# Performance work log

Hardware: AMD Instinct MI355X
Metric: run time of the kernel (lower is better)

The kernel has to match this reference:

```python
import jax, jax.numpy as jnp
import numpy as np


def setup_inputs() -> dict:
    key = jax.random.key(0)
    ks = jax.random.split(key, 5)
    B, T, S, D = 4, 32, 320, 768
    return {
        "x": jax.random.normal(ks[0], (B, T, S, D), dtype=jnp.float32),
        "qkv_w": jax.random.normal(ks[1], (D, 3 * D), dtype=jnp.float32) * 0.02,
        "qkv_b": jax.random.normal(ks[2], (3 * D,), dtype=jnp.float32) * 0.02,
        "out_w": jax.random.normal(ks[3], (D, D), dtype=jnp.float32) * 0.02,
        "out_b": jax.random.normal(ks[4], (D,), dtype=jnp.float32) * 0.02,
        "n_latents": 64,
        "n_heads": 12,
    }


def reference(x, qkv_w, qkv_b, out_w, out_b, n_latents, n_heads):
    B, T, S, D = x.shape
    H = n_heads
    hd = D // H
    scale = 1.0 / jnp.sqrt(jnp.asarray(hd, dtype=x.dtype))

    # qkv projection: [B,T,S,3D]
    qkv = jnp.einsum('btsd,de->btse', x, qkv_w) + qkv_b
    q, k, v = jnp.split(qkv, 3, axis=-1)
    # [B,T,S,H,hd]
    q = q.reshape(B, T, S, H, hd)
    k = k.reshape(B, T, S, H, hd)
    v = v.reshape(B, T, S, H, hd)

    # block-sparse mask: latent queries (rows < n_latents) cannot attend to
    # patch keys (cols >= n_latents); everything else allowed
    rows = jnp.arange(S) < n_latents          # latent query rows
    cols = jnp.arange(S) >= n_latents         # patch key cols
    allow = ~(rows[:, None] & cols[None, :])  # [S,S] bool

    # attention scores [B,T,H,Sq,Sk]
    scores = jnp.einsum('btqhd,btkhd->bthqk', q, k) * scale
    scores = jnp.where(allow, scores, -jnp.inf)
    attn = jax.nn.softmax(scores, axis=-1)

    y = jnp.einsum('bthqk,btkhd->btqhd', attn, v).reshape(B, T, S, D)
    return jnp.einsum('btsd,de->btse', y, out_w) + out_b
```

## Files before the change

kernel.cpp:

```cpp
#include <hip/hip_runtime.h>

typedef __attribute__((ext_vector_type(8))) short bf16x8;
typedef __attribute__((ext_vector_type(4))) float f32x4;
typedef __attribute__((ext_vector_type(16))) float f32x16;
typedef __attribute__((address_space(1))) void gvoid_t;
typedef __attribute__((address_space(3))) void lvoid_t;

#define DEVI __device__ __forceinline__

DEVI unsigned short f2bf(float f) {
    unsigned int u = __builtin_bit_cast(unsigned int, f);
    u += 0x7fffu + ((u >> 16) & 1u);
    return (unsigned short)(u >> 16);
}

DEVI unsigned cvt_pk_bf16(float a, float b) {
    unsigned r;
    asm("v_cvt_pk_bf16_f32 %0, %1, %2" : "=v"(r) : "v"(a), "v"(b));
    return r;
}

DEVI f32x4 mfma16(bf16x8 a, bf16x8 b, f32x4 c) {
    return __builtin_amdgcn_mfma_f32_16x16x32_bf16(a, b, c, 0, 0, 0);
}

__global__ void k_convert(const float* __restrict__ in, unsigned short* __restrict__ out, int n8) {
    int i = blockIdx.x * 256 + threadIdx.x;
    if (i >= n8) return;
    const float4* p = (const float4*)in + (size_t)i * 2;
    float4 a = p[0], b = p[1];
    uint4 o;
    o.x = f2bf(a.x) | ((unsigned)f2bf(a.y) << 16);
    o.y = f2bf(a.z) | ((unsigned)f2bf(a.w) << 16);
    o.z = f2bf(b.x) | ((unsigned)f2bf(b.y) << 16);
    o.w = f2bf(b.z) | ((unsigned)f2bf(b.w) << 16);
    *((uint4*)out + i) = o;
}

__global__ void k_transpose(const float* __restrict__ w, unsigned short* __restrict__ wt, int K, int N) {
    __shared__ float tile[32][33];
    int n0 = blockIdx.x * 32, k0 = blockIdx.y * 32;
    int tx = threadIdx.x, ty = threadIdx.y;
#pragma unroll
    for (int r = 0; r < 32; r += 8)
        tile[ty + r][tx] = w[(size_t)(k0 + ty + r) * N + n0 + tx];
    __syncthreads();
#pragma unroll
    for (int r = 0; r < 32; r += 8)
        wt[(size_t)(n0 + ty + r) * K + k0 + tx] = f2bf(tile[tx][ty + r]);
}

template <bool OUT_BF16>
__global__ __launch_bounds__(512, 2) void k_gemm256(const unsigned short* __restrict__ A,
                                                    const unsigned short* __restrict__ Bt,
                                                    const float* __restrict__ bias,
                                                    void* __restrict__ out,
                                                    int M, int N, int K) {
    __shared__ unsigned short smem[65536];

    const int tid = threadIdx.x;
    const int nwg = gridDim.x, bid = blockIdx.x;
    const int q8 = nwg >> 3, r8 = nwg & 7;
    const int xcd = bid & 7, lid = bid >> 3;
    const int swz = ((xcd < r8) ? xcd * (q8 + 1) : r8 * (q8 + 1) + (xcd - r8) * q8) + lid;
    const int ntn = N >> 8;
    const int bm = swz / ntn, bn = swz % ntn;

    const int lane = tid & 63, wid = tid >> 6;
    const int wr = wid >> 2, wc = wid & 3;
    const int lr = lane & 15, lg = lane >> 4;
    const int cswz = (lr & 7) << 3;
    const int col0 = (lg * 8) ^ cswz;

    const int NT = K >> 6;

    const int srowl = tid >> 3;
    const int scole = ((tid & 7) ^ (srowl & 7)) << 3;
    const unsigned short* aSrc = A  + (size_t)(bm * 256 + srowl) * K + scole;
    const unsigned short* bSrc = Bt + (size_t)(bn * 256 + srowl) * K + scole;

#define STG(matOff, srcBase, qq, koff, bufw)                                              \
    __builtin_amdgcn_global_load_lds((gvoid_t*)((srcBase) + (size_t)(qq) * 64 * K + (koff)), \
        (lvoid_t*)(smem + (matOff) + (bufw) * 16384 + (qq) * 4096 + tid * 8), 16, 0, 0)

    f32x4 acc[8][4];
#pragma unroll
    for (int i = 0; i < 8; ++i)
#pragma unroll
        for (int j = 0; j < 4; ++j) acc[i][j] = (f32x4){0.f, 0.f, 0.f, 0.f};

    {
        const int k1 = (NT > 1) ? 64 : 0;
        STG(0, aSrc, 0, 0, 0); STG(0, aSrc, 1, 0, 0); STG(0, aSrc, 2, 0, 0); STG(0, aSrc, 3, 0, 0);
        STG(32768, bSrc, 0, 0, 0); STG(32768, bSrc, 1, 0, 0); STG(32768, bSrc, 2, 0, 0); STG(32768, bSrc, 3, 0, 0);
        STG(0, aSrc, 0, k1, 1); STG(0, aSrc, 2, k1, 1);
        asm volatile("s_waitcnt vmcnt(2)" ::: "memory");
        __builtin_amdgcn_s_barrier();
    }

#pragma unroll 1
    for (int t = 0; t < NT; ++t) {
        const int bufR = t & 1, bufW = bufR ^ 1;
        const int ko1 = (t + 1 < NT) ? (t + 1) * 64 : 0;
        const int ko2 = (t + 2 < NT) ? (t + 2) * 64 : 0;
        const unsigned short* abuf = smem + bufR * 16384;
        const unsigned short* bbuf = smem + 32768 + bufR * 16384;
        bf16x8 af[4][2], b01[2][2], b23[2][2];

#pragma unroll
        for (int mf = 0; mf < 4; ++mf)
#pragma unroll
            for (int kk = 0; kk < 2; ++kk)
                af[mf][kk] = *(const bf16x8*)(abuf + (wr * 128 + mf * 16 + lr) * 64 + (col0 ^ (kk * 32)));
#pragma unroll
        for (int j = 0; j < 2; ++j)
#pragma unroll
            for (int kk = 0; kk < 2; ++kk)
                b01[j][kk] = *(const bf16x8*)(bbuf + (wc * 64 + j * 16 + lr) * 64 + (col0 ^ (kk * 32)));
        STG(32768, bSrc, 0, ko1, bufW); STG(32768, bSrc, 1, ko1, bufW);
        __builtin_amdgcn_s_barrier();
        asm volatile("s_waitcnt lgkmcnt(0)" ::: "memory");
        __builtin_amdgcn_sched_barrier(0);
        __builtin_amdgcn_s_setprio(1);
#pragma unroll
        for (int mf = 0; mf < 4; ++mf)
#pragma unroll
            for (int j = 0; j < 2; ++j)
#pragma unroll
                for (int kk = 0; kk < 2; ++kk)
                    acc[mf][j] = mfma16(af[mf][kk], b01[j][kk], acc[mf][j]);
        __builtin_amdgcn_s_setprio(0);
        __builtin_amdgcn_s_barrier();

#pragma unroll
        for (int j = 0; j < 2; ++j)
#pragma unroll
            for (int kk = 0; kk < 2; ++kk)
                b23[j][kk] = *(const bf16x8*)(bbuf + (wc * 64 + (2 + j) * 16 + lr) * 64 + (col0 ^ (kk * 32)));
        STG(32768, bSrc, 2, ko1, bufW); STG(32768, bSrc, 3, ko1, bufW);
        __builtin_amdgcn_s_barrier();
        asm volatile("s_waitcnt lgkmcnt(0)" ::: "memory");
        __builtin_amdgcn_sched_barrier(0);
        __builtin_amdgcn_s_setprio(1);
#pragma unroll
        for (int mf = 0; mf < 4; ++mf)
#pragma unroll
            for (int j = 0; j < 2; ++j)
#pragma unroll
                for (int kk = 0; kk < 2; ++kk)
                    acc[mf][2 + j] = mfma16(af[mf][kk], b23[j][kk], acc[mf][2 + j]);
        __builtin_amdgcn_s_setprio(0);
        __builtin_amdgcn_s_barrier();

#pragma unroll
        for (int mf = 0; mf < 4; ++mf)
#pragma unroll
            for (int kk = 0; kk < 2; ++kk)
                af[mf][kk] = *(const bf16x8*)(abuf + (wr * 128 + 64 + mf * 16 + lr) * 64 + (col0 ^ (kk * 32)));
        STG(0, aSrc, 1, ko1, bufW); STG(0, aSrc, 3, ko1, bufW);
        __builtin_amdgcn_s_barrier();
        asm volatile("s_waitcnt lgkmcnt(0)" ::: "memory");
        __builtin_amdgcn_sched_barrier(0);
        __builtin_amdgcn_s_setprio(1);
#pragma unroll
        for (int mf = 0; mf < 4; ++mf)
#pragma unroll
            for (int j = 0; j < 2; ++j)
#pragma unroll
                for (int kk = 0; kk < 2; ++kk)
                    acc[4 + mf][2 + j] = mfma16(af[mf][kk], b23[j][kk], acc[4 + mf][2 + j]);
        __builtin_amdgcn_s_setprio(0);
        __builtin_amdgcn_s_barrier();

        STG(0, aSrc, 0, ko2, bufR); STG(0, aSrc, 2, ko2, bufR);
        __builtin_amdgcn_s_setprio(1);
#pragma unroll
        for (int mf = 0; mf < 4; ++mf)
#pragma unroll
            for (int j = 0; j < 2; ++j)
#pragma unroll
                for (int kk = 0; kk < 2; ++kk)
                    acc[4 + mf][j] = mfma16(af[mf][kk], b01[j][kk], acc[4 + mf][j]);
        __builtin_amdgcn_s_setprio(0);
        asm volatile("s_waitcnt vmcnt(2)" ::: "memory");
        __builtin_amdgcn_s_barrier();
    }
#undef STG

    asm volatile("s_waitcnt vmcnt(0)" ::: "memory");
    float bv[4];
#pragma unroll
    for (int nf = 0; nf < 4; ++nf)
        bv[nf] = bias[bn * 256 + wc * 64 + nf * 16 + lr];

    if (OUT_BF16) {
        unsigned short* ebuf = smem + wid * 8192;
#pragma unroll
        for (int h = 0; h < 2; ++h) {
#pragma unroll
            for (int mf4 = 0; mf4 < 4; ++mf4) {
                int mf = h * 4 + mf4;
#pragma unroll
                for (int nf = 0; nf < 4; ++nf)
#pragma unroll
                    for (int i = 0; i < 4; ++i)
                        ebuf[(mf4 * 16 + lg * 4 + i) * 72 + nf * 16 + lr] = f2bf(acc[mf][nf][i] + bv[nf]);
            }
            asm volatile("s_waitcnt lgkmcnt(0)" ::: "memory");
            __builtin_amdgcn_sched_barrier(0);
#pragma unroll
            for (int ps = 0; ps < 8; ++ps) {
                int rl = ps * 8 + (lane >> 3), ck = lane & 7;
                uint4 vv = *(const uint4*)&ebuf[rl * 72 + ck * 8];
                int grow = bm * 256 + wr * 128 + h * 64 + rl;
                int gcol = bn * 256 + wc * 64 + ck * 8;
                *(uint4*)&((unsigned short*)out)[(size_t)grow * N + gcol] = vv;
            }
            asm volatile("s_waitcnt lgkmcnt(0)" ::: "memory");
            __builtin_amdgcn_sched_barrier(0);
        }
    } else {
        float* ebuf = (float*)smem + wid * 4096;
#pragma unroll
        for (int qq = 0; qq < 4; ++qq) {
#pragma unroll
            for (int m2 = 0; m2 < 2; ++m2) {
                int mf = qq * 2 + m2;
#pragma unroll
                for (int nf = 0; nf < 4; ++nf)
#pragma unroll
                    for (int i = 0; i < 4; ++i)
                        ebuf[(m2 * 16 + lg * 4 + i) * 68 + nf * 16 + lr] = acc[mf][nf][i] + bv[nf];
            }
            asm volatile("s_waitcnt lgkmcnt(0)" ::: "memory");
            __builtin_amdgcn_sched_barrier(0);
#pragma unroll
            for (int ps = 0; ps < 8; ++ps) {
                int rl = ps * 4 + (lane >> 4), ck = lane & 15;
                uint4 vv = *(const uint4*)&ebuf[rl * 68 + ck * 4];
                int grow = bm * 256 + wr * 128 + qq * 32 + rl;
                int gcol = bn * 256 + wc * 64 + ck * 4;
                *(uint4*)&((float*)out)[(size_t)grow * N + gcol] = vv;
            }
            asm volatile("s_waitcnt lgkmcnt(0)" ::: "memory");
            __builtin_amdgcn_sched_barrier(0);
        }
    }
}

__global__ __launch_bounds__(640) void k_attn4(const unsigned short* __restrict__ qkv,
                                               unsigned short* __restrict__ y) {
    int bt = blockIdx.x / 12, h = blockIdx.x % 12;
    const unsigned short* Qg = qkv + (size_t)bt * 320 * 2304 + h * 64;
    const unsigned short* Kg = Qg + 768;
    const unsigned short* Vg = Qg + 1536;

    __shared__ unsigned short Vt[10 * 64 * 40];

    int tid = threadIdx.x, w = tid >> 6, l = tid & 63;
    int q = l & 31, hh = l >> 5;
    int q0 = w * 32;
    int ntile = (w < 2) ? 2 : 10;

    {
        int k = tid >> 1;
        int tt = k >> 5, sk = k & 31;
        int d0 = (tid & 1) * 32;
        const unsigned short* src = Vg + (size_t)k * 2304 + d0;
#pragma unroll
        for (int c = 0; c < 4; ++c) {
            union { uint4 u; unsigned short s[8]; } vv;
            vv.u = *(const uint4*)(src + c * 8);
#pragma unroll
            for (int j = 0; j < 8; ++j) {
                int d = d0 + c * 8 + j;
                Vt[(tt * 64 + d) * 40 + (sk ^ (((d >> 3) & 3) << 3))] = vv.s[j];
            }
        }
    }

    bf16x8 qf[4];
#pragma unroll
    for (int c = 0; c < 4; ++c)
        qf[c] = *(const bf16x8*)(Qg + (size_t)(q0 + q) * 2304 + c * 16 + hh * 8);

    f32x16 o0 = (f32x16)0.f, o1 = (f32x16)0.f;
    float m = -3e38f, lsum = 0.f;
    const float SC = 0.125f * 1.44269504089f;

    bf16x8 kfA[4], kfB[4];
    auto loadK = [&](bf16x8 (&kf)[4], int tt) {
#pragma unroll
        for (int c = 0; c < 4; ++c)
            kf[c] = *(const bf16x8*)(Kg + (size_t)(tt * 32 + q) * 2304 + c * 16 + hh * 8);
    };
    loadK(kfA, 0);

    __syncthreads();

    auto process = [&](int t, bf16x8 (&kf)[4]) {
        f32x16 sacc = (f32x16)0.f;
#pragma unroll
        for (int c = 0; c < 4; ++c)
            sacc = __builtin_amdgcn_mfma_f32_32x32x16_bf16(kf[c], qf[c], sacc, 0, 0, 0);

        float p[16];
#pragma unroll
        for (int r = 0; r < 16; ++r) p[r] = sacc[r] * SC;
        float tm = fmaxf(
            fmaxf(fmaxf(fmaxf(p[0], p[1]), fmaxf(p[2], p[3])),
                  fmaxf(fmaxf(p[4], p[5]), fmaxf(p[6], p[7]))),
            fmaxf(fmaxf(fmaxf(p[8], p[9]), fmaxf(p[10], p[11])),
                  fmaxf(fmaxf(p[12], p[13]), fmaxf(p[14], p[15]))));
        tm = fmaxf(tm, __shfl_xor(tm, 32));
        if (!__all(tm <= m + 8.f)) {
            float mn = fmaxf(m, tm);
            float al = __builtin_amdgcn_exp2f(m - mn);
            lsum *= al;
#pragma unroll
            for (int r = 0; r < 16; ++r) { o0[r] *= al; o1[r] *= al; }
            m = mn;
        }
#pragma unroll
        for (int r = 0; r < 16; ++r) p[r] = __builtin_amdgcn_exp2f(p[r] - m);
        float rs =
            ((p[0] + p[1]) + (p[2] + p[3])) + ((p[4] + p[5]) + (p[6] + p[7])) +
            (((p[8] + p[9]) + (p[10] + p[11])) + ((p[12] + p[13]) + (p[14] + p[15])));
        lsum += rs;

        unsigned a0 = cvt_pk_bf16(p[0], p[1]);
        unsigned a1 = cvt_pk_bf16(p[2], p[3]);
        unsigned b0 = cvt_pk_bf16(p[4], p[5]);
        unsigned b1 = cvt_pk_bf16(p[6], p[7]);
        asm("v_permlane32_swap_b32 %0, %1" : "+v"(a0), "+v"(b0));
        asm("v_permlane32_swap_b32 %0, %1" : "+v"(a1), "+v"(b1));
        unsigned c0 = cvt_pk_bf16(p[8], p[9]);
        unsigned c1 = cvt_pk_bf16(p[10], p[11]);
        unsigned d0 = cvt_pk_bf16(p[12], p[13]);
        unsigned d1 = cvt_pk_bf16(p[14], p[15]);
        asm("v_permlane32_swap_b32 %0, %1" : "+v"(c0), "+v"(d0));
        asm("v_permlane32_swap_b32 %0, %1" : "+v"(c1), "+v"(d1));
        union { unsigned u[4]; bf16x8 v; } pf0, pf1;
        pf0.u[0] = a0; pf0.u[1] = a1; pf0.u[2] = b0; pf0.u[3] = b1;
        pf1.u[0] = c0; pf1.u[1] = c1; pf1.u[2] = d0; pf1.u[3] = d1;

        const unsigned short* vt = Vt + t * 2560;
        {
            int d = q;
            int sw = (d >> 3) & 3;
            bf16x8 va0 = *(const bf16x8*)&vt[d * 40 + ((0 + hh) ^ sw) * 8];
            bf16x8 va1 = *(const bf16x8*)&vt[d * 40 + ((2 + hh) ^ sw) * 8];
            o0 = __builtin_amdgcn_mfma_f32_32x32x16_bf16(va0, pf0.v, o0, 0, 0, 0);
            o0 = __builtin_amdgcn_mfma_f32_32x32x16_bf16(va1, pf1.v, o0, 0, 0, 0);
        }
        {
            int d = 32 + q;
            int sw = (d >> 3) & 3;
            bf16x8 va0 = *(const bf16x8*)&vt[d * 40 + ((0 + hh) ^ sw) * 8];
            bf16x8 va1 = *(const bf16x8*)&vt[d * 40 + ((2 + hh) ^ sw) * 8];
            o1 = __builtin_amdgcn_mfma_f32_32x32x16_bf16(va0, pf0.v, o1, 0, 0, 0);
            o1 = __builtin_amdgcn_mfma_f32_32x32x16_bf16(va1, pf1.v, o1, 0, 0, 0);
        }
    };

    for (int t = 0; t < ntile; t += 2) {
        loadK(kfB, t + 1);
        process(t, kfA);
        loadK(kfA, (t + 2 < 10) ? (t + 2) : 8);
        process(t + 1, kfB);
    }

    lsum += __shfl_xor(lsum, 32);
    float inv = 1.f / lsum;
    unsigned short* yp = y + (size_t)(bt * 320 + q0 + q) * 768 + h * 64;
#pragma unroll
    for (int r = 0; r < 16; r += 2) {
        int dr = (r & 3) + 8 * (r >> 2) + 4 * hh;
        *(unsigned*)(yp + dr) =
            (unsigned)f2bf(o0[r] * inv) | ((unsigned)f2bf(o0[r + 1] * inv) << 16);
        *(unsigned*)(yp + 32 + dr) =
            (unsigned)f2bf(o1[r] * inv) | ((unsigned)f2bf(o1[r + 1] * inv) << 16);
    }
}

extern "C" void kernel_launch(void* const* d_in, const int* in_sizes, int n_in,
                              void* d_out, int out_size, void* d_ws, size_t ws_size,
                              hipStream_t stream) {
    const float* x     = (const float*)d_in[0];
    const float* qkv_w = (const float*)d_in[1];
    const float* qkv_b = (const float*)d_in[2];
    const float* out_w = (const float*)d_in[3];
    const float* out_b = (const float*)d_in[4];

    const int M = 40960;
    unsigned short* xb  = (unsigned short*)d_ws;
    unsigned short* w1t = xb + (size_t)M * 768;
    unsigned short* w2t = w1t + (size_t)2304 * 768;
    unsigned short* qkv = w2t + (size_t)768 * 768;
    unsigned short* yb  = qkv + (size_t)M * 2304;

    k_convert<<<(M * 768 / 8 + 255) / 256, 256, 0, stream>>>(x, xb, M * 768 / 8);
    k_transpose<<<dim3(2304 / 32, 768 / 32), dim3(32, 8), 0, stream>>>(qkv_w, w1t, 768, 2304);
    k_transpose<<<dim3(768 / 32, 768 / 32), dim3(32, 8), 0, stream>>>(out_w, w2t, 768, 768);

    k_gemm256<true><<<(M / 256) * (2304 / 256), 512, 0, stream>>>(xb, w1t, qkv_b, (void*)qkv, M, 2304, 768);
    k_attn4<<<128 * 12, 640, 0, stream>>>(qkv, yb);
    k_gemm256<false><<<(M / 256) * (768 / 256), 512, 0, stream>>>(yb, w2t, out_b, d_out, M, 768, 768);
}
```

Before: 378.6 us.

## Drop mid-loop barriers in GEMM and prepack K tiles for attention

The GEMM main loop no longer places a workgroup barrier between each MFMA quarter. It splits the LDS fragment loads into halves with partial lgkmcnt waits, so MFMAs can start while the remaining fragments arrive, and it keeps a single vmcnt(0) plus barrier at the end of each iteration. A new k_kpack kernel copies K into a per-(bt,head,tile) contiguous layout in the now-unused x buffer, so the attention kernel's K fragment loads become contiguous 16-byte loads instead of loads strided by 2304. This trades an extra launch and roughly 60MB of extra memory traffic for better-coalesced K reads and fewer GEMM synchronisations. The stricter vmcnt(0) wait also reduces prefetch overlap slightly.

```diff
diff --git a/kernel.cpp b/kernel.cpp
--- a/kernel.cpp
+++ b/kernel.cpp
@@ -7,6 +7,7 @@
 typedef __attribute__((address_space(3))) void lvoid_t;
 
 #define DEVI __device__ __forceinline__
+#define SB __builtin_amdgcn_sched_barrier(0)
 
 DEVI unsigned short f2bf(float f) {
     unsigned int u = __builtin_bit_cast(unsigned int, f);
@@ -50,6 +51,18 @@
         wt[(size_t)(n0 + ty + r) * K + k0 + tx] = f2bf(tile[tx][ty + r]);
 }
 
+__global__ __launch_bounds__(256) void k_kpack(const unsigned short* __restrict__ qkv,
+                                               unsigned short* __restrict__ kp) {
+    int bht = blockIdx.x;
+    int t = bht % 10, bh = bht / 10;
+    int h = bh % 12, bt = bh / 12;
+    int c = threadIdx.x >> 6, l = threadIdx.x & 63;
+    const unsigned short* src = qkv + (size_t)(bt * 320 + t * 32 + (l & 31)) * 2304
+                                + 768 + h * 64 + c * 16 + (l >> 5) * 8;
+    uint4 v = *(const uint4*)src;
+    *(uint4*)(kp + ((size_t)bht * 4 + c) * 512 + l * 8) = v;
+}
+
 template <bool OUT_BF16>
 __global__ __launch_bounds__(512, 2) void k_gemm256(const unsigned short* __restrict__ A,
                                                     const unsigned short* __restrict__ Bt,
@@ -82,6 +95,8 @@
 #define STG(matOff, srcBase, qq, koff, bufw)                                              \
     __builtin_amdgcn_global_load_lds((gvoid_t*)((srcBase) + (size_t)(qq) * 64 * K + (koff)), \
         (lvoid_t*)(smem + (matOff) + (bufw) * 16384 + (qq) * 4096 + tid * 8), 16, 0, 0)
+#define LDA(mf, base, rowoff, kk) \
+    *(const bf16x8*)((base) + ((rowoff) + (mf) * 16 + lr) * 64 + (col0 ^ ((kk) * 32)))
 
     f32x4 acc[8][4];
 #pragma unroll
@@ -105,89 +120,125 @@
         const int ko2 = (t + 2 < NT) ? (t + 2) * 64 : 0;
         const unsigned short* abuf = smem + bufR * 16384;
         const unsigned short* bbuf = smem + 32768 + bufR * 16384;
-        bf16x8 af[4][2], b01[2][2], b23[2][2];
-
+        bf16x8 afv[4][2], b01[2][2], b23[2][2];
+
+#pragma unroll
+        for (int j = 0; j < 2; ++j)
+#pragma unroll
+            for (int kk = 0; kk < 2; ++kk)
+                b01[j][kk] = LDA(j, bbuf, wc * 64, kk);
+#pragma unroll
+        for (int mf = 0; mf < 2; ++mf)
+#pragma unroll
+            for (int kk = 0; kk < 2; ++kk)
+                afv[mf][kk] = LDA(mf, abuf, wr * 128, kk);
+        SB;
+#pragma unroll
+        for (int mf = 2; mf < 4; ++mf)
+#pragma unroll
+            for (int kk = 0; kk < 2; ++kk)
+                afv[mf][kk] = LDA(mf, abuf, wr * 128, kk);
+        SB;
+        STG(32768, bSrc, 0, ko1, bufW); STG(32768, bSrc, 1, ko1, bufW);
+        asm volatile("s_waitcnt lgkmcnt(4)" ::: "memory"); SB;
+        __builtin_amdgcn_s_setprio(1);
+#pragma unroll
+        for (int mf = 0; mf < 2; ++mf)
+#pragma unroll
+            for (int j = 0; j < 2; ++j)
+#pragma unroll
+                for (int kk = 0; kk < 2; ++kk)
+                    acc[mf][j] = mfma16(afv[mf][kk], b01[j][kk], acc[mf][j]);
+        __builtin_amdgcn_s_setprio(0);
+        asm volatile("s_waitcnt lgkmcnt(0)" ::: "memory"); SB;
+        __builtin_amdgcn_s_setprio(1);
+#pragma unroll
+        for (int mf = 2; mf < 4; ++mf)
+#pragma unroll
+            for (int j = 0; j < 2; ++j)
+#pragma unroll
+                for (int kk = 0; kk < 2; ++kk)
+                    acc[mf][j] = mfma16(afv[mf][kk], b01[j][kk], acc[mf][j]);
+        __builtin_amdgcn_s_setprio(0);
+
+#pragma unroll
+        for (int kk = 0; kk < 2; ++kk)
+            b23[0][kk] = LDA(2, bbuf, wc * 64, kk);
+        SB;
+#pragma unroll
+        for (int kk = 0; kk < 2; ++kk)
+            b23[1][kk] = LDA(3, bbuf, wc * 64, kk);
+        SB;
+        STG(32768, bSrc, 2, ko1, bufW); STG(32768, bSrc, 3, ko1, bufW);
+        asm volatile("s_waitcnt lgkmcnt(2)" ::: "memory"); SB;
+        __builtin_amdgcn_s_setprio(1);
 #pragma unroll
         for (int mf = 0; mf < 4; ++mf)
 #pragma unroll
             for (int kk = 0; kk < 2; ++kk)
-                af[mf][kk] = *(const bf16x8*)(abuf + (wr * 128 + mf * 16 + lr) * 64 + (col0 ^ (kk * 32)));
-#pragma unroll
-        for (int j = 0; j < 2; ++j)
-#pragma unroll
-            for (int kk = 0; kk < 2; ++kk)
-                b01[j][kk] = *(const bf16x8*)(bbuf + (wc * 64 + j * 16 + lr) * 64 + (col0 ^ (kk * 32)));
-        STG(32768, bSrc, 0, ko1, bufW); STG(32768, bSrc, 1, ko1, bufW);
+                acc[mf][2] = mfma16(afv[mf][kk], b23[0][kk], acc[mf][2]);
+        __builtin_amdgcn_s_setprio(0);
+        asm volatile("s_waitcnt lgkmcnt(0)" ::: "memory"); SB;
+        __builtin_amdgcn_s_setprio(1);
+#pragma unroll
+        for (int mf = 0; mf < 4; ++mf)
+#pragma unroll
+            for (int kk = 0; kk < 2; ++kk)
+                acc[mf][3] = mfma16(afv[mf][kk], b23[1][kk], acc[mf][3]);
+        __builtin_amdgcn_s_setprio(0);
+
+#pragma unroll
+        for (int mf = 0; mf < 2; ++mf)
+#pragma unroll
+            for (int kk = 0; kk < 2; ++kk)
+                afv[mf][kk] = LDA(mf, abuf, wr * 128 + 64, kk);
+        SB;
+#pragma unroll
+        for (int mf = 2; mf < 4; ++mf)
+#pragma unroll
+            for (int kk = 0; kk < 2; ++kk)
+                afv[mf][kk] = LDA(mf, abuf, wr * 128 + 64, kk);
+        SB;
+        STG(0, aSrc, 1, ko1, bufW); STG(0, aSrc, 3, ko1, bufW);
+        asm volatile("s_waitcnt lgkmcnt(4)" ::: "memory"); SB;
+        __builtin_amdgcn_s_setprio(1);
+#pragma unroll
+        for (int mf = 0; mf < 2; ++mf)
+#pragma unroll
+            for (int j = 0; j < 2; ++j)
+#pragma unroll
+                for (int kk = 0; kk < 2; ++kk)
+                    acc[4 + mf][2 + j] = mfma16(afv[mf][kk], b23[j][kk], acc[4 + mf][2 + j]);
+        __builtin_amdgcn_s_setprio(0);
+        asm volatile("s_waitcnt lgkmcnt(0)" ::: "memory"); SB;
+        __builtin_amdgcn_s_setprio(1);
+#pragma unroll
+        for (int mf = 2; mf < 4; ++mf)
+#pragma unroll
+            for (int j = 0; j < 2; ++j)
+#pragma unroll
+                for (int kk = 0; kk < 2; ++kk)
+                    acc[4 + mf][2 + j] = mfma16(afv[mf][kk], b23[j][kk], acc[4 + mf][2 + j]);
+        __builtin_amdgcn_s_setprio(0);
+
+        __builtin_amdgcn_s_setprio(1);
+#pragma unroll
+        for (int mf = 0; mf < 4; ++mf)
+#pragma unroll
+            for (int j = 0; j < 2; ++j)
+#pragma unroll
+                for (int kk = 0; kk < 2; ++kk)
+                    acc[4 + mf][j] = mfma16(afv[mf][kk], b01[j][kk], acc[4 + mf][j]);
+        __builtin_amdgcn_s_setprio(0);
+        asm volatile("s_waitcnt vmcnt(0)" ::: "memory");
         __builtin_amdgcn_s_barrier();
-        asm volatile("s_waitcnt lgkmcnt(0)" ::: "memory");
-        __builtin_amdgcn_sched_barrier(0);
-        __builtin_amdgcn_s_setprio(1);
-#pragma unroll
-        for (int mf = 0; mf < 4; ++mf)
-#pragma unroll
-            for (int j = 0; j < 2; ++j)
-#pragma unroll
-                for (int kk = 0; kk < 2; ++kk)
-                    acc[mf][j] = mfma16(af[mf][kk], b01[j][kk], acc[mf][j]);
-        __builtin_amdgcn_s_setprio(0);
-        __builtin_amdgcn_s_barrier();
-
-#pragma unroll
-        for (int j = 0; j < 2; ++j)
-#pragma unroll
-            for (int kk = 0; kk < 2; ++kk)
-                b23[j][kk] = *(const bf16x8*)(bbuf + (wc * 64 + (2 + j) * 16 + lr) * 64 + (col0 ^ (kk * 32)));
-        STG(32768, bSrc, 2, ko1, bufW); STG(32768, bSrc, 3, ko1, bufW);
-        __builtin_amdgcn_s_barrier();
-        asm volatile("s_waitcnt lgkmcnt(0)" ::: "memory");
-        __builtin_amdgcn_sched_barrier(0);
-        __builtin_amdgcn_s_setprio(1);
-#pragma unroll
-        for (int mf = 0; mf < 4; ++mf)
-#pragma unroll
-            for (int j = 0; j < 2; ++j)
-#pragma unroll
-                for (int kk = 0; kk < 2; ++kk)
-                    acc[mf][2 + j] = mfma16(af[mf][kk], b23[j][kk], acc[mf][2 + j]);
-        __builtin_amdgcn_s_setprio(0);
-        __builtin_amdgcn_s_barrier();
-
-#pragma unroll
-        for (int mf = 0; mf < 4; ++mf)
-#pragma unroll
-            for (int kk = 0; kk < 2; ++kk)
-                af[mf][kk] = *(const bf16x8*)(abuf + (wr * 128 + 64 + mf * 16 + lr) * 64 + (col0 ^ (kk * 32)));
-        STG(0, aSrc, 1, ko1, bufW); STG(0, aSrc, 3, ko1, bufW);
-        __builtin_amdgcn_s_barrier();
-        asm volatile("s_waitcnt lgkmcnt(0)" ::: "memory");
-        __builtin_amdgcn_sched_barrier(0);
-        __builtin_amdgcn_s_setprio(1);
-#pragma unroll
-        for (int mf = 0; mf < 4; ++mf)
-#pragma unroll
-            for (int j = 0; j < 2; ++j)
-#pragma unroll
-                for (int kk = 0; kk < 2; ++kk)
-                    acc[4 + mf][2 + j] = mfma16(af[mf][kk], b23[j][kk], acc[4 + mf][2 + j]);
-        __builtin_amdgcn_s_setprio(0);
-        __builtin_amdgcn_s_barrier();
-
         STG(0, aSrc, 0, ko2, bufR); STG(0, aSrc, 2, ko2, bufR);
-        __builtin_amdgcn_s_setprio(1);
-#pragma unroll
-        for (int mf = 0; mf < 4; ++mf)
-#pragma unroll
-            for (int j = 0; j < 2; ++j)
-#pragma unroll
-                for (int kk = 0; kk < 2; ++kk)
-                    acc[4 + mf][j] = mfma16(af[mf][kk], b01[j][kk], acc[4 + mf][j]);
-        __builtin_amdgcn_s_setprio(0);
-        asm volatile("s_waitcnt vmcnt(2)" ::: "memory");
-        __builtin_amdgcn_s_barrier();
     }
 #undef STG
+#undef LDA
 
     asm volatile("s_waitcnt vmcnt(0)" ::: "memory");
+    __syncthreads();
     float bv[4];
 #pragma unroll
     for (int nf = 0; nf < 4; ++nf)
@@ -206,8 +257,7 @@
                     for (int i = 0; i < 4; ++i)
                         ebuf[(mf4 * 16 + lg * 4 + i) * 72 + nf * 16 + lr] = f2bf(acc[mf][nf][i] + bv[nf]);
             }
-            asm volatile("s_waitcnt lgkmcnt(0)" ::: "memory");
-            __builtin_amdgcn_sched_barrier(0);
+            asm volatile("s_waitcnt lgkmcnt(0)" ::: "memory"); SB;
 #pragma unroll
             for (int ps = 0; ps < 8; ++ps) {
                 int rl = ps * 8 + (lane >> 3), ck = lane & 7;
@@ -216,8 +266,7 @@
                 int gcol = bn * 256 + wc * 64 + ck * 8;
                 *(uint4*)&((unsigned short*)out)[(size_t)grow * N + gcol] = vv;
             }
-            asm volatile("s_waitcnt lgkmcnt(0)" ::: "memory");
-            __builtin_amdgcn_sched_barrier(0);
+            asm volatile("s_waitcnt lgkmcnt(0)" ::: "memory"); SB;
         }
     } else {
         float* ebuf = (float*)smem + wid * 4096;
@@ -232,8 +281,7 @@
                     for (int i = 0; i < 4; ++i)
                         ebuf[(m2 * 16 + lg * 4 + i) * 68 + nf * 16 + lr] = acc[mf][nf][i] + bv[nf];
             }
-            asm volatile("s_waitcnt lgkmcnt(0)" ::: "memory");
-            __builtin_amdgcn_sched_barrier(0);
+            asm volatile("s_waitcnt lgkmcnt(0)" ::: "memory"); SB;
 #pragma unroll
             for (int ps = 0; ps < 8; ++ps) {
                 int rl = ps * 4 + (lane >> 4), ck = lane & 15;
@@ -242,18 +290,18 @@
                 int gcol = bn * 256 + wc * 64 + ck * 4;
                 *(uint4*)&((float*)out)[(size_t)grow * N + gcol] = vv;
             }
-            asm volatile("s_waitcnt lgkmcnt(0)" ::: "memory");
-            __builtin_amdgcn_sched_barrier(0);
-        }
-    }
-}
-
-__global__ __launch_bounds__(640) void k_attn4(const unsigned short* __restrict__ qkv,
+            asm volatile("s_waitcnt lgkmcnt(0)" ::: "memory"); SB;
+        }
+    }
+}
+
+__global__ __launch_bounds__(640) void k_attn5(const unsigned short* __restrict__ qkv,
+                                               const unsigned short* __restrict__ kp,
                                                unsigned short* __restrict__ y) {
     int bt = blockIdx.x / 12, h = blockIdx.x % 12;
     const unsigned short* Qg = qkv + (size_t)bt * 320 * 2304 + h * 64;
-    const unsigned short* Kg = Qg + 768;
     const unsigned short* Vg = Qg + 1536;
+    const unsigned short* Kpb = kp + (size_t)blockIdx.x * 20480;
 
     __shared__ unsigned short Vt[10 * 64 * 40];
 
@@ -292,7 +340,7 @@
     auto loadK = [&](bf16x8 (&kf)[4], int tt) {
 #pragma unroll
         for (int c = 0; c < 4; ++c)
-            kf[c] = *(const bf16x8*)(Kg + (size_t)(tt * 32 + q) * 2304 + c * 16 + hh * 8);
+            kf[c] = *(const bf16x8*)(Kpb + tt * 2048 + c * 512 + l * 8);
     };
     loadK(kfA, 0);
 
@@ -398,12 +446,14 @@
     unsigned short* w2t = w1t + (size_t)2304 * 768;
     unsigned short* qkv = w2t + (size_t)768 * 768;
     unsigned short* yb  = qkv + (size_t)M * 2304;
+    unsigned short* kp  = xb;
 
     k_convert<<<(M * 768 / 8 + 255) / 256, 256, 0, stream>>>(x, xb, M * 768 / 8);
     k_transpose<<<dim3(2304 / 32, 768 / 32), dim3(32, 8), 0, stream>>>(qkv_w, w1t, 768, 2304);
     k_transpose<<<dim3(768 / 32, 768 / 32), dim3(32, 8), 0, stream>>>(out_w, w2t, 768, 768);
 
     k_gemm256<true><<<(M / 256) * (2304 / 256), 512, 0, stream>>>(xb, w1t, qkv_b, (void*)qkv, M, 2304, 768);
-    k_attn4<<<128 * 12, 640, 0, stream>>>(qkv, yb);
+    k_kpack<<<1536 * 10, 256, 0, stream>>>(qkv, kp);
+    k_attn5<<<128 * 12, 640, 0, stream>>>(qkv, kp, yb);
     k_gemm256<false><<<(M / 256) * (768 / 256), 512, 0, stream>>>(yb, w2t, out_b, d_out, M, 768, 768);
 }
```

Measured after the change: 378.3 us. Within noise of the previous version (-0.1%).
